# Kernel tuning notes

Hardware: AMD Instinct MI355X
Metric: run time of the kernel (lower is better)

## Reference

```python
import jax, jax.numpy as jnp
import numpy as np

B, S, D, H = 4, 2048, 1024, 16
HD = D // H  # 64


def setup_inputs() -> dict:
    key = jax.random.key(0)
    ks = jax.random.split(key, 9)
    s = 1.0 / np.sqrt(D)
    return {
        "x": jax.random.normal(ks[0], (B, S, D), dtype=jnp.float32),
        "Wq": jax.random.normal(ks[1], (D, D), dtype=jnp.float32) * s,
        "bq": jax.random.normal(ks[2], (D,), dtype=jnp.float32) * 0.01,
        "Wk": jax.random.normal(ks[3], (D, D), dtype=jnp.float32) * s,
        "bk": jax.random.normal(ks[4], (D,), dtype=jnp.float32) * 0.01,
        "Wv": jax.random.normal(ks[5], (D, D), dtype=jnp.float32) * s,
        "bv": jax.random.normal(ks[6], (D,), dtype=jnp.float32) * 0.01,
        "Wo": jax.random.normal(ks[7], (D, D), dtype=jnp.float32) * s,
        "bo": jax.random.normal(ks[8], (D,), dtype=jnp.float32) * 0.01,
    }


def reference(x, Wq, bq, Wk, bk, Wv, bv, Wo, bo):
    b, s, _ = x.shape
    # projections -> [b, h, s, hd]
    def proj(W, bias):
        return (x @ W.T + bias).reshape(b, s, H, HD).transpose(0, 2, 1, 3)
    q, k, v = proj(Wq, bq), proj(Wk, bk), proj(Wv, bv)
    # NOTE: source multiplies by sqrt(head_dim)**0.5 = head_dim**0.25 (quirk kept)
    scale = jnp.asarray(HD, dtype=x.dtype) ** 0.25
    scores = jnp.einsum("bhqd,bhkd->bhqk", q, k) * scale
    causal = jnp.tril(jnp.ones((s, s), dtype=bool))
    scores = jnp.where(causal, scores, -jnp.inf)
    attn = jax.nn.softmax(scores, axis=-1)  # dropout p=0 (eval) -> identity
    out = jnp.einsum("bhqk,bhkd->bhqd", attn, v)
    out = out.transpose(0, 2, 1, 3).reshape(b, s, D)
    return out @ Wo.T + bo
```

## Files before the change

kernel.cpp:

```cpp
#include <hip/hip_runtime.h>
#include <hip/hip_fp16.h>


typedef unsigned short u16;
typedef _Float16 half8 __attribute__((ext_vector_type(8)));
typedef float f32x4 __attribute__((ext_vector_type(4)));
typedef unsigned short ushort8 __attribute__((ext_vector_type(8)));

#define LOG2E 1.4426950408889634f
#define ATTN_SCALE 2.8284271247461903f
#define SWZ(r) ((((r) ^ ((r) >> 3))) & 7)

__device__ __forceinline__ u16 f2h(float f) {
  return __half_as_ushort(__float2half(f));
}

__device__ __forceinline__ void gload16(const void* gsrc, void* ldst) {
  typedef __attribute__((address_space(1))) const void glob_t;
  typedef __attribute__((address_space(3))) void lds_t;
  __builtin_amdgcn_global_load_lds((glob_t*)gsrc, (lds_t*)ldst, 16, 0, 0);
}

__device__ __forceinline__ f32x4 mfma_f16(half8 a, half8 b, f32x4 c) {
  return __builtin_amdgcn_mfma_f32_16x16x32_f16(a, b, c, 0, 0, 0);
}

__global__ __launch_bounds__(256) void cvt_f32_f16(const float* __restrict__ in,
                                                   u16* __restrict__ out, int n8) {
  int i = blockIdx.x * 256 + threadIdx.x;
  if (i >= n8) return;
  const float4* p = (const float4*)in + (size_t)i * 2;
  float4 a = p[0], b = p[1];
  ushort8 v;
  v[0] = f2h(a.x); v[1] = f2h(a.y); v[2] = f2h(a.z); v[3] = f2h(a.w);
  v[4] = f2h(b.x); v[5] = f2h(b.y); v[6] = f2h(b.z); v[7] = f2h(b.w);
  *(ushort8*)(out + (size_t)i * 8) = v;
}

__device__ __forceinline__ void gemm_body(const u16* __restrict__ A, const u16* __restrict__ Bw,
                                          const float* __restrict__ bias,
                                          u16* __restrict__ Ch, float* __restrict__ Cf) {
  __shared__ __align__(16) u16 sA[128 * 32];
  __shared__ __align__(16) u16 sB[128 * 32];
  const int m0 = blockIdx.y * 128, n0 = blockIdx.x * 128;
  const int tid = threadIdx.x, w = tid >> 6, l = tid & 63;
  const int wm = (w >> 1) * 64, wn = (w & 1) * 64;
  f32x4 acc[4][4] = {};
  const int srow = tid >> 2, sch = (tid & 3) * 8;
  char* sAb = (char*)sA + w * 1024;
  char* sBb = (char*)sB + w * 1024;
  const u16* Ag0 = A + (size_t)(m0 + srow) * 1024 + sch;
  const u16* Ag1 = A + (size_t)(m0 + 64 + srow) * 1024 + sch;
  const u16* Bg0 = Bw + (size_t)(n0 + srow) * 1024 + sch;
  const u16* Bg1 = Bw + (size_t)(n0 + 64 + srow) * 1024 + sch;
  for (int kt = 0; kt < 32; ++kt) {
    const int k0 = kt * 32;
    __syncthreads();
    gload16(Ag0 + k0, sAb);
    gload16(Ag1 + k0, sAb + 4096);
    gload16(Bg0 + k0, sBb);
    gload16(Bg1 + k0, sBb + 4096);
    __syncthreads();
    half8 a[4], b[4];
#pragma unroll
    for (int mf = 0; mf < 4; ++mf)
      a[mf] = *(const half8*)&sA[(wm + mf * 16 + (l & 15)) * 32 + (l >> 4) * 8];
#pragma unroll
    for (int nf = 0; nf < 4; ++nf)
      b[nf] = *(const half8*)&sB[(wn + nf * 16 + (l & 15)) * 32 + (l >> 4) * 8];
#pragma unroll
    for (int mf = 0; mf < 4; ++mf)
#pragma unroll
      for (int nf = 0; nf < 4; ++nf)
        acc[mf][nf] = mfma_f16(a[mf], b[nf], acc[mf][nf]);
  }
#pragma unroll
  for (int nf = 0; nf < 4; ++nf) {
    const int col = n0 + wn + nf * 16 + (l & 15);
    const float bv = bias[col];
#pragma unroll
    for (int mf = 0; mf < 4; ++mf) {
#pragma unroll
      for (int r = 0; r < 4; ++r) {
        const int row = m0 + wm + mf * 16 + (l >> 4) * 4 + r;
        float v = acc[mf][nf][r] + bv;
        if (Cf) Cf[(size_t)row * 1024 + col] = v;
        else    Ch[(size_t)row * 1024 + col] = f2h(v);
      }
    }
  }
}

struct QkvArgs {
  const u16* B[3];
  const float* bias[3];
  u16* C[3];
};

__global__ __launch_bounds__(256) void gemm_qkv(const u16* __restrict__ A, QkvArgs ga) {
  const int z = blockIdx.z;
  gemm_body(A, ga.B[z], ga.bias[z], ga.C[z], nullptr);
}

__global__ __launch_bounds__(256) void gemm_out(const u16* __restrict__ A, const u16* __restrict__ Bw,
                                                const float* __restrict__ bias, float* __restrict__ C) {
  gemm_body(A, Bw, bias, nullptr, C);
}

__global__ __launch_bounds__(256) void attn_fused(const u16* __restrict__ Qb, const u16* __restrict__ Kb,
                                                  const u16* __restrict__ Vb, u16* __restrict__ Ob) {
  __shared__ __align__(16) u16 q_s[64 * 64];
  __shared__ __align__(16) u16 k_s[64 * 64];
  __shared__ __align__(16) u16 vt_s[64 * 64];
  __shared__ __align__(16) u16 p_s[4 * 16 * 64];
  const int bid = blockIdx.x;
  const int bh = bid & 63;
  const int qt = 31 - (bid >> 6);
  const int b = bh >> 4, h = bh & 15;
  const size_t base = (size_t)b * 2048 * 1024 + h * 64;
  const int q0 = qt * 64;
  const int tid = threadIdx.x, w = tid >> 6, l = tid & 63;

  {
    const int row0 = w * 8 + (l >> 3), ch = l & 7;
#pragma unroll
    for (int is = 0; is < 2; ++is) {
      const int row = is * 32 + row0;
      const int sch = ch ^ SWZ(row);
      gload16(Qb + base + (size_t)(q0 + row) * 1024 + sch * 8, (char*)q_s + is * 4096 + w * 1024);
    }
  }
  f32x4 o[4] = {};
  float m_r[4], l_r[4];
#pragma unroll
  for (int r = 0; r < 4; ++r) { m_r[r] = -INFINITY; l_r[r] = 0.f; }

  for (int kt = 0; kt <= qt; ++kt) {
    __syncthreads();
    {
      const int row0 = w * 8 + (l >> 3), ch = l & 7;
#pragma unroll
      for (int is = 0; is < 2; ++is) {
        const int row = is * 32 + row0;
        const int sch = ch ^ SWZ(row);
        gload16(Kb + base + (size_t)(kt * 64 + row) * 1024 + sch * 8, (char*)k_s + is * 4096 + w * 1024);
      }
    }
#pragma unroll
    for (int rr = 0; rr < 2; ++rr) {
      const int k = rr * 32 + (tid >> 3);
      const int d0 = (tid & 7) * 8;
      ushort8 vv = *(const ushort8*)(Vb + base + (size_t)(kt * 64 + k) * 1024 + d0);
#pragma unroll
      for (int j = 0; j < 8; ++j) {
        const int d = d0 + j;
        vt_s[d * 64 + (((k >> 3) ^ SWZ(d)) << 3) + (k & 7)] = vv[j];
      }
    }
    __syncthreads();
    f32x4 s[4] = {};
#pragma unroll
    for (int st = 0; st < 2; ++st) {
      const int ch = st * 4 + (l >> 4);
      const int qrow = w * 16 + (l & 15);
      half8 aq = *(const half8*)&q_s[qrow * 64 + ((ch ^ SWZ(qrow)) << 3)];
#pragma unroll
      for (int nf = 0; nf < 4; ++nf) {
        const int krow = nf * 16 + (l & 15);
        half8 bk = *(const half8*)&k_s[krow * 64 + ((ch ^ SWZ(krow)) << 3)];
        s[nf] = mfma_f16(aq, bk, s[nf]);
      }
    }
#pragma unroll
    for (int nf = 0; nf < 4; ++nf)
#pragma unroll
      for (int r = 0; r < 4; ++r) s[nf][r] *= ATTN_SCALE;
    if (kt == qt) {
#pragma unroll
      for (int nf = 0; nf < 4; ++nf) {
        const int kc = nf * 16 + (l & 15);
#pragma unroll
        for (int r = 0; r < 4; ++r) {
          const int qr = w * 16 + (l >> 4) * 4 + r;
          if (kc > qr) s[nf][r] = -INFINITY;
        }
      }
    }
#pragma unroll
    for (int r = 0; r < 4; ++r) {
      float t = fmaxf(fmaxf(s[0][r], s[1][r]), fmaxf(s[2][r], s[3][r]));
      t = fmaxf(t, __shfl_xor(t, 1));
      t = fmaxf(t, __shfl_xor(t, 2));
      t = fmaxf(t, __shfl_xor(t, 4));
      t = fmaxf(t, __shfl_xor(t, 8));
      const float mn = fmaxf(m_r[r], t);
      const float al = exp2f((m_r[r] - mn) * LOG2E);
      float rs = 0.f;
#pragma unroll
      for (int nf = 0; nf < 4; ++nf) {
        const float p = exp2f((s[nf][r] - mn) * LOG2E);
        s[nf][r] = p;
        rs += p;
      }
      rs += __shfl_xor(rs, 1);
      rs += __shfl_xor(rs, 2);
      rs += __shfl_xor(rs, 4);
      rs += __shfl_xor(rs, 8);
      l_r[r] = l_r[r] * al + rs;
      m_r[r] = mn;
#pragma unroll
      for (int nf2 = 0; nf2 < 4; ++nf2) o[nf2][r] *= al;
    }
    u16* pw = p_s + w * 1024;
#pragma unroll
    for (int nf = 0; nf < 4; ++nf) {
      const int col = nf * 16 + (l & 15);
      const int cch = col >> 3, clo = col & 7;
#pragma unroll
      for (int r = 0; r < 4; ++r) {
        const int row = (l >> 4) * 4 + r;
        pw[row * 64 + ((cch ^ SWZ(row)) << 3) + clo] = f2h(s[nf][r]);
      }
    }
#pragma unroll
    for (int ks = 0; ks < 2; ++ks) {
      const int prow = l & 15;
      const int ch = ks * 4 + (l >> 4);
      half8 pa = *(const half8*)&pw[prow * 64 + ((ch ^ SWZ(prow)) << 3)];
#pragma unroll
      for (int nf2 = 0; nf2 < 4; ++nf2) {
        const int vrow = nf2 * 16 + (l & 15);
        half8 vb = *(const half8*)&vt_s[vrow * 64 + ((ch ^ SWZ(vrow)) << 3)];
        o[nf2] = mfma_f16(pa, vb, o[nf2]);
      }
    }
  }
#pragma unroll
  for (int nf2 = 0; nf2 < 4; ++nf2) {
    const int col = nf2 * 16 + (l & 15);
#pragma unroll
    for (int r = 0; r < 4; ++r) {
      const int row = q0 + w * 16 + (l >> 4) * 4 + r;
      Ob[base + (size_t)row * 1024 + col] = f2h(o[nf2][r] / l_r[r]);
    }
  }
}

extern "C" void kernel_launch(void* const* d_in, const int* in_sizes, int n_in,
                              void* d_out, int out_size, void* d_ws, size_t ws_size,
                              hipStream_t stream) {
  (void)in_sizes; (void)n_in; (void)out_size; (void)ws_size;
  const float* x  = (const float*)d_in[0];
  const float* Wq = (const float*)d_in[1];
  const float* bq = (const float*)d_in[2];
  const float* Wk = (const float*)d_in[3];
  const float* bk = (const float*)d_in[4];
  const float* Wv = (const float*)d_in[5];
  const float* bv = (const float*)d_in[6];
  const float* Wo = (const float*)d_in[7];
  const float* bo = (const float*)d_in[8];

  u16* xb = (u16*)d_ws;
  u16* wq = xb + (size_t)8192 * 1024;
  u16* wk = wq + 1024 * 1024;
  u16* wv = wk + 1024 * 1024;
  u16* wo = wv + 1024 * 1024;
  u16* Qb = wo + 1024 * 1024;
  u16* Kb = Qb + (size_t)8192 * 1024;
  u16* Vb = Kb + (size_t)8192 * 1024;
  u16* Ab = xb;

  cvt_f32_f16<<<4096, 256, 0, stream>>>(x, xb, 1048576);
  cvt_f32_f16<<<512, 256, 0, stream>>>(Wq, wq, 131072);
  cvt_f32_f16<<<512, 256, 0, stream>>>(Wk, wk, 131072);
  cvt_f32_f16<<<512, 256, 0, stream>>>(Wv, wv, 131072);
  cvt_f32_f16<<<512, 256, 0, stream>>>(Wo, wo, 131072);

  QkvArgs ga;
  ga.B[0] = wq; ga.B[1] = wk; ga.B[2] = wv;
  ga.bias[0] = bq; ga.bias[1] = bk; ga.bias[2] = bv;
  ga.C[0] = Qb; ga.C[1] = Kb; ga.C[2] = Vb;
  gemm_qkv<<<dim3(8, 64, 3), 256, 0, stream>>>(xb, ga);

  attn_fused<<<2048, 256, 0, stream>>>(Qb, Kb, Vb, Ab);

  gemm_out<<<dim3(8, 64), 256, 0, stream>>>(Ab, wo, bo, (float*)d_out);
}
```

Measured before the change: 346.3 us.

## Write V transposed from QKV GEMM and restructure attention to compute S^T

The QKV GEMM epilogue now writes V in a per-head transposed layout, so the attention kernel can async-load V^T tiles straight into LDS instead of scalar-transposing them each iteration. The attention kernel keeps Q fragments in registers, drops the Q LDS buffer, and swaps the MFMA operand order so each lane owns one query row. That turns the row max and sum reductions into two cross-lane shuffles and lets P be written and O stored as 4-element vectors. The scale is folded into a log2e-premultiplied constant and the raw exp2 builtin is used. The risk is that the strided transposed epilogue stores in the GEMM are less coalesced.

```diff
diff --git a/kernel.cpp b/kernel.cpp
--- a/kernel.cpp
+++ b/kernel.cpp
@@ -6,9 +6,10 @@
 typedef _Float16 half8 __attribute__((ext_vector_type(8)));
 typedef float f32x4 __attribute__((ext_vector_type(4)));
 typedef unsigned short ushort8 __attribute__((ext_vector_type(8)));
+typedef unsigned short us4 __attribute__((ext_vector_type(4)));
 
 #define LOG2E 1.4426950408889634f
-#define ATTN_SCALE 2.8284271247461903f
+#define SCL2 4.0816663172343815f
 #define SWZ(r) ((((r) ^ ((r) >> 3))) & 7)
 
 __device__ __forceinline__ u16 f2h(float f) {
@@ -39,7 +40,8 @@
 
 __device__ __forceinline__ void gemm_body(const u16* __restrict__ A, const u16* __restrict__ Bw,
                                           const float* __restrict__ bias,
-                                          u16* __restrict__ Ch, float* __restrict__ Cf) {
+                                          u16* __restrict__ Ch, float* __restrict__ Cf,
+                                          u16* __restrict__ Vtp) {
   __shared__ __align__(16) u16 sA[128 * 32];
   __shared__ __align__(16) u16 sB[128 * 32];
   const int m0 = blockIdx.y * 128, n0 = blockIdx.x * 128;
@@ -74,18 +76,35 @@
       for (int nf = 0; nf < 4; ++nf)
         acc[mf][nf] = mfma_f16(a[mf], b[nf], acc[mf][nf]);
   }
-#pragma unroll
-  for (int nf = 0; nf < 4; ++nf) {
-    const int col = n0 + wn + nf * 16 + (l & 15);
-    const float bv = bias[col];
-#pragma unroll
-    for (int mf = 0; mf < 4; ++mf) {
-#pragma unroll
-      for (int r = 0; r < 4; ++r) {
-        const int row = m0 + wm + mf * 16 + (l >> 4) * 4 + r;
-        float v = acc[mf][nf][r] + bv;
-        if (Cf) Cf[(size_t)row * 1024 + col] = v;
-        else    Ch[(size_t)row * 1024 + col] = f2h(v);
+  if (Vtp) {
+#pragma unroll
+    for (int nf = 0; nf < 4; ++nf) {
+      const int col = n0 + wn + nf * 16 + (l & 15);
+      const float bv = bias[col];
+#pragma unroll
+      for (int mf = 0; mf < 4; ++mf) {
+        const int row = m0 + wm + mf * 16 + (l >> 4) * 4;
+        us4 v;
+#pragma unroll
+        for (int r = 0; r < 4; ++r) v[r] = f2h(acc[mf][nf][r] + bv);
+        *(us4*)(Vtp + (size_t)((row >> 11) * 16 + (col >> 6)) * 131072 +
+                (size_t)(col & 63) * 2048 + (row & 2047)) = v;
+      }
+    }
+  } else {
+#pragma unroll
+    for (int nf = 0; nf < 4; ++nf) {
+      const int col = n0 + wn + nf * 16 + (l & 15);
+      const float bv = bias[col];
+#pragma unroll
+      for (int mf = 0; mf < 4; ++mf) {
+#pragma unroll
+        for (int r = 0; r < 4; ++r) {
+          const int row = m0 + wm + mf * 16 + (l >> 4) * 4 + r;
+          float v = acc[mf][nf][r] + bv;
+          if (Cf) Cf[(size_t)row * 1024 + col] = v;
+          else    Ch[(size_t)row * 1024 + col] = f2h(v);
+        }
       }
     }
   }
@@ -99,17 +118,17 @@
 
 __global__ __launch_bounds__(256) void gemm_qkv(const u16* __restrict__ A, QkvArgs ga) {
   const int z = blockIdx.z;
-  gemm_body(A, ga.B[z], ga.bias[z], ga.C[z], nullptr);
+  if (z == 2) gemm_body(A, ga.B[2], ga.bias[2], nullptr, nullptr, ga.C[2]);
+  else        gemm_body(A, ga.B[z], ga.bias[z], ga.C[z], nullptr, nullptr);
 }
 
 __global__ __launch_bounds__(256) void gemm_out(const u16* __restrict__ A, const u16* __restrict__ Bw,
                                                 const float* __restrict__ bias, float* __restrict__ C) {
-  gemm_body(A, Bw, bias, nullptr, C);
+  gemm_body(A, Bw, bias, nullptr, C, nullptr);
 }
 
 __global__ __launch_bounds__(256) void attn_fused(const u16* __restrict__ Qb, const u16* __restrict__ Kb,
-                                                  const u16* __restrict__ Vb, u16* __restrict__ Ob) {
-  __shared__ __align__(16) u16 q_s[64 * 64];
+                                                  const u16* __restrict__ Vt, u16* __restrict__ Ob) {
   __shared__ __align__(16) u16 k_s[64 * 64];
   __shared__ __align__(16) u16 vt_s[64 * 64];
   __shared__ __align__(16) u16 p_s[4 * 16 * 64];
@@ -117,132 +136,122 @@
   const int bh = bid & 63;
   const int qt = 31 - (bid >> 6);
   const int b = bh >> 4, h = bh & 15;
-  const size_t base = (size_t)b * 2048 * 1024 + h * 64;
+  const size_t baseQ = (size_t)b * 2048 * 1024 + h * 64;
+  const size_t baseV = (size_t)(b * 16 + h) * 131072;
   const int q0 = qt * 64;
   const int tid = threadIdx.x, w = tid >> 6, l = tid & 63;
-
+  const int g = l >> 4, qi = l & 15;
+  const int q_loc = w * 16 + qi;
+  const int q_glob = q0 + q_loc;
+
+  half8 qf0, qf1;
   {
-    const int row0 = w * 8 + (l >> 3), ch = l & 7;
-#pragma unroll
-    for (int is = 0; is < 2; ++is) {
-      const int row = is * 32 + row0;
-      const int sch = ch ^ SWZ(row);
-      gload16(Qb + base + (size_t)(q0 + row) * 1024 + sch * 8, (char*)q_s + is * 4096 + w * 1024);
-    }
-  }
-  f32x4 o[4] = {};
-  float m_r[4], l_r[4];
-#pragma unroll
-  for (int r = 0; r < 4; ++r) { m_r[r] = -INFINITY; l_r[r] = 0.f; }
+    const u16* qp = Qb + baseQ + (size_t)q_glob * 1024 + g * 8;
+    qf0 = *(const half8*)(qp);
+    qf1 = *(const half8*)(qp + 32);
+  }
+  const int srow = w * 8 + (l >> 3);
+  const int sch0 = (l & 7) ^ SWZ(srow);
+  const int sch1 = (l & 7) ^ SWZ(srow + 32);
+  const u16* pK0 = Kb + baseQ + (size_t)srow * 1024 + sch0 * 8;
+  const u16* pK1 = Kb + baseQ + (size_t)(srow + 32) * 1024 + sch1 * 8;
+  const u16* pV0 = Vt + baseV + (size_t)srow * 2048 + sch0 * 8;
+  const u16* pV1 = Vt + baseV + (size_t)(srow + 32) * 2048 + sch1 * 8;
+  char* kd0 = (char*)k_s + w * 1024;
+  char* kd1 = (char*)k_s + 4096 + w * 1024;
+  char* vd0 = (char*)vt_s + w * 1024;
+  char* vd1 = (char*)vt_s + 4096 + w * 1024;
+  int koff[4], pvoff[2];
+#pragma unroll
+  for (int nf = 0; nf < 4; ++nf) {
+    const int row = nf * 16 + qi;
+    koff[nf] = row * 64 + ((g ^ SWZ(row)) << 3);
+  }
+#pragma unroll
+  for (int ks = 0; ks < 2; ++ks)
+    pvoff[ks] = qi * 64 + (((ks * 4 + g) ^ SWZ(qi)) << 3);
+  u16* pw = p_s + w * 1024;
+
+  f32x4 s[4], o[4] = {};
+  float m_r = -INFINITY, l_r = 0.f;
 
   for (int kt = 0; kt <= qt; ++kt) {
     __syncthreads();
-    {
-      const int row0 = w * 8 + (l >> 3), ch = l & 7;
-#pragma unroll
-      for (int is = 0; is < 2; ++is) {
-        const int row = is * 32 + row0;
-        const int sch = ch ^ SWZ(row);
-        gload16(Kb + base + (size_t)(kt * 64 + row) * 1024 + sch * 8, (char*)k_s + is * 4096 + w * 1024);
-      }
-    }
-#pragma unroll
-    for (int rr = 0; rr < 2; ++rr) {
-      const int k = rr * 32 + (tid >> 3);
-      const int d0 = (tid & 7) * 8;
-      ushort8 vv = *(const ushort8*)(Vb + base + (size_t)(kt * 64 + k) * 1024 + d0);
-#pragma unroll
-      for (int j = 0; j < 8; ++j) {
-        const int d = d0 + j;
-        vt_s[d * 64 + (((k >> 3) ^ SWZ(d)) << 3) + (k & 7)] = vv[j];
-      }
-    }
-    __syncthreads();
-    f32x4 s[4] = {};
-#pragma unroll
-    for (int st = 0; st < 2; ++st) {
-      const int ch = st * 4 + (l >> 4);
-      const int qrow = w * 16 + (l & 15);
-      half8 aq = *(const half8*)&q_s[qrow * 64 + ((ch ^ SWZ(qrow)) << 3)];
+    gload16(pK0, kd0);
+    gload16(pK1, kd1);
+    gload16(pV0, vd0);
+    gload16(pV1, vd1);
+    pK0 += 65536; pK1 += 65536; pV0 += 64; pV1 += 64;
+    __syncthreads();
+#pragma unroll
+    for (int nf = 0; nf < 4; ++nf) {
+      half8 k0 = *(const half8*)(k_s + koff[nf]);
+      half8 k1 = *(const half8*)(k_s + (koff[nf] ^ 32));
+      f32x4 acc = {};
+      acc = mfma_f16(k0, qf0, acc);
+      acc = mfma_f16(k1, qf1, acc);
+      s[nf] = acc * SCL2;
+    }
+    if (kt == qt) {
 #pragma unroll
       for (int nf = 0; nf < 4; ++nf) {
-        const int krow = nf * 16 + (l & 15);
-        half8 bk = *(const half8*)&k_s[krow * 64 + ((ch ^ SWZ(krow)) << 3)];
-        s[nf] = mfma_f16(aq, bk, s[nf]);
-      }
-    }
-#pragma unroll
-    for (int nf = 0; nf < 4; ++nf)
-#pragma unroll
-      for (int r = 0; r < 4; ++r) s[nf][r] *= ATTN_SCALE;
-    if (kt == qt) {
-#pragma unroll
-      for (int nf = 0; nf < 4; ++nf) {
-        const int kc = nf * 16 + (l & 15);
-#pragma unroll
-        for (int r = 0; r < 4; ++r) {
-          const int qr = w * 16 + (l >> 4) * 4 + r;
-          if (kc > qr) s[nf][r] = -INFINITY;
-        }
-      }
-    }
-#pragma unroll
-    for (int r = 0; r < 4; ++r) {
-      float t = fmaxf(fmaxf(s[0][r], s[1][r]), fmaxf(s[2][r], s[3][r]));
-      t = fmaxf(t, __shfl_xor(t, 1));
-      t = fmaxf(t, __shfl_xor(t, 2));
-      t = fmaxf(t, __shfl_xor(t, 4));
-      t = fmaxf(t, __shfl_xor(t, 8));
-      const float mn = fmaxf(m_r[r], t);
-      const float al = exp2f((m_r[r] - mn) * LOG2E);
-      float rs = 0.f;
-#pragma unroll
-      for (int nf = 0; nf < 4; ++nf) {
-        const float p = exp2f((s[nf][r] - mn) * LOG2E);
+        const int kb = nf * 16 + g * 4;
+#pragma unroll
+        for (int r = 0; r < 4; ++r)
+          if (kb + r > q_loc) s[nf][r] = -INFINITY;
+      }
+    }
+    float t = fmaxf(fmaxf(fmaxf(s[0][0], s[0][1]), fmaxf(s[0][2], s[0][3])),
+                    fmaxf(fmaxf(s[1][0], s[1][1]), fmaxf(s[1][2], s[1][3])));
+    t = fmaxf(t, fmaxf(fmaxf(fmaxf(s[2][0], s[2][1]), fmaxf(s[2][2], s[2][3])),
+                       fmaxf(fmaxf(s[3][0], s[3][1]), fmaxf(s[3][2], s[3][3]))));
+    t = fmaxf(t, __shfl_xor(t, 16));
+    t = fmaxf(t, __shfl_xor(t, 32));
+    const float mn = fmaxf(m_r, t);
+    const float al = __builtin_amdgcn_exp2f(m_r - mn);
+    float rs = 0.f;
+#pragma unroll
+    for (int nf = 0; nf < 4; ++nf) {
+#pragma unroll
+      for (int r = 0; r < 4; ++r) {
+        const float p = __builtin_amdgcn_exp2f(s[nf][r] - mn);
         s[nf][r] = p;
         rs += p;
       }
-      rs += __shfl_xor(rs, 1);
-      rs += __shfl_xor(rs, 2);
-      rs += __shfl_xor(rs, 4);
-      rs += __shfl_xor(rs, 8);
-      l_r[r] = l_r[r] * al + rs;
-      m_r[r] = mn;
-#pragma unroll
-      for (int nf2 = 0; nf2 < 4; ++nf2) o[nf2][r] *= al;
-    }
-    u16* pw = p_s + w * 1024;
-#pragma unroll
-    for (int nf = 0; nf < 4; ++nf) {
-      const int col = nf * 16 + (l & 15);
-      const int cch = col >> 3, clo = col & 7;
-#pragma unroll
-      for (int r = 0; r < 4; ++r) {
-        const int row = (l >> 4) * 4 + r;
-        pw[row * 64 + ((cch ^ SWZ(row)) << 3) + clo] = f2h(s[nf][r]);
-      }
+    }
+    rs += __shfl_xor(rs, 16);
+    rs += __shfl_xor(rs, 32);
+    l_r = l_r * al + rs;
+    m_r = mn;
+#pragma unroll
+    for (int nf = 0; nf < 4; ++nf) o[nf] *= al;
+#pragma unroll
+    for (int nf = 0; nf < 4; ++nf) {
+      us4 v;
+      v[0] = f2h(s[nf][0]); v[1] = f2h(s[nf][1]);
+      v[2] = f2h(s[nf][2]); v[3] = f2h(s[nf][3]);
+      const int c = nf * 2 + (g >> 1);
+      *(us4*)(pw + qi * 64 + ((c ^ SWZ(qi)) << 3) + (g & 1) * 4) = v;
     }
 #pragma unroll
     for (int ks = 0; ks < 2; ++ks) {
-      const int prow = l & 15;
-      const int ch = ks * 4 + (l >> 4);
-      half8 pa = *(const half8*)&pw[prow * 64 + ((ch ^ SWZ(prow)) << 3)];
-#pragma unroll
-      for (int nf2 = 0; nf2 < 4; ++nf2) {
-        const int vrow = nf2 * 16 + (l & 15);
-        half8 vb = *(const half8*)&vt_s[vrow * 64 + ((ch ^ SWZ(vrow)) << 3)];
-        o[nf2] = mfma_f16(pa, vb, o[nf2]);
-      }
-    }
-  }
-#pragma unroll
-  for (int nf2 = 0; nf2 < 4; ++nf2) {
-    const int col = nf2 * 16 + (l & 15);
-#pragma unroll
-    for (int r = 0; r < 4; ++r) {
-      const int row = q0 + w * 16 + (l >> 4) * 4 + r;
-      Ob[base + (size_t)row * 1024 + col] = f2h(o[nf2][r] / l_r[r]);
-    }
+      half8 pf = *(const half8*)(pw + pvoff[ks]);
+#pragma unroll
+      for (int nf = 0; nf < 4; ++nf) {
+        const int vrow = nf * 16 + qi;
+        half8 vf = *(const half8*)(vt_s + vrow * 64 + (((ks * 4 + g) ^ SWZ(vrow)) << 3));
+        o[nf] = mfma_f16(vf, pf, o[nf]);
+      }
+    }
+  }
+  const float inv = 1.f / l_r;
+  u16* op = Ob + (size_t)(b * 2048 + q_glob) * 1024 + h * 64 + g * 4;
+#pragma unroll
+  for (int nf = 0; nf < 4; ++nf) {
+    us4 v;
+#pragma unroll
+    for (int r = 0; r < 4; ++r) v[r] = f2h(o[nf][r] * inv);
+    *(us4*)(op + nf * 16) = v;
   }
 }
 
@@ -267,7 +276,7 @@
   u16* wo = wv + 1024 * 1024;
   u16* Qb = wo + 1024 * 1024;
   u16* Kb = Qb + (size_t)8192 * 1024;
-  u16* Vb = Kb + (size_t)8192 * 1024;
+  u16* Vt = Kb + (size_t)8192 * 1024;
   u16* Ab = xb;
 
   cvt_f32_f16<<<4096, 256, 0, stream>>>(x, xb, 1048576);
@@ -279,10 +288,10 @@
   QkvArgs ga;
   ga.B[0] = wq; ga.B[1] = wk; ga.B[2] = wv;
   ga.bias[0] = bq; ga.bias[1] = bk; ga.bias[2] = bv;
-  ga.C[0] = Qb; ga.C[1] = Kb; ga.C[2] = Vb;
+  ga.C[0] = Qb; ga.C[1] = Kb; ga.C[2] = Vt;
   gemm_qkv<<<dim3(8, 64, 3), 256, 0, stream>>>(xb, ga);
 
-  attn_fused<<<2048, 256, 0, stream>>>(Qb, Kb, Vb, Ab);
+  attn_fused<<<2048, 256, 0, stream>>>(Qb, Kb, Vt, Ab);
 
   gemm_out<<<dim3(8, 64), 256, 0, stream>>>(Ab, wo, bo, (float*)d_out);
 }
```

Measured after the change: 302.7 us. 1.14x faster.
